# Optimization experiments

Hardware: AMD Instinct MI355X
Metric: run time of the kernel (lower is better)

## Reference

```python
import jax, jax.numpy as jnp
import numpy as np

NUM_TOKENS = 8192
D_MODEL = 512
D_FF = 1024
NUM_EXPERTS = 8
TOP_K = 2


def setup_inputs() -> dict:
    key = jax.random.key(0)
    k_x, k_r, k_w1, k_w2 = jax.random.split(key, 4)
    x = jax.random.normal(k_x, (NUM_TOKENS, D_MODEL), dtype=jnp.float32)
    # Router weight [num_experts, d_model]
    w_router = jax.random.normal(k_r, (NUM_EXPERTS, D_MODEL), dtype=jnp.float32) * 0.02
    # Expert weights stored as [E, N, K] (kernel convention: y = x @ W.T)
    w1 = jax.random.normal(k_w1, (NUM_EXPERTS, D_FF, D_MODEL), dtype=jnp.float32) * 0.02
    w2 = jax.random.normal(k_w2, (NUM_EXPERTS, D_MODEL, D_FF), dtype=jnp.float32) * 0.02
    return {"x": x, "w_router": w_router, "w1": w1, "w2": w2}


def reference(x, w_router, w1, w2):
    # Router: softmax over experts, top-k selection, renormalized gates
    logits = jnp.einsum("td,ed->te", x, w_router)            # [T, E]
    probs = jax.nn.softmax(logits, axis=-1)
    top_vals, top_idx = jax.lax.top_k(probs, TOP_K)           # [T, k]
    top_vals = top_vals / jnp.sum(top_vals, axis=-1, keepdims=True)

    # Combine weights per (token, expert): topk weight if selected else 0.
    # out[t] = sum_e gate[t,e] * W2[e] @ silu(W1[e] @ x[t])
    out = jnp.zeros_like(x)
    for e in range(NUM_EXPERTS):
        gate_e = jnp.sum(jnp.where(top_idx == e, top_vals, 0.0), axis=-1)  # [T]
        h = jax.nn.silu(jnp.einsum("td,fd->tf", x, w1[e]))                 # [T, d_ff]
        y = jnp.einsum("tf,df->td", h, w2[e])                              # [T, d]
        out = out + gate_e[:, None] * y
    return out
```

## Files before the change

### kernel.cpp

```cpp
#include <hip/hip_runtime.h>
#include <hip/hip_bf16.h>

#define NT 8192
#define DM 512
#define DF 1024
#define NE 8
#define MAXROWS (NT*2)

typedef __bf16 bf16_8 __attribute__((ext_vector_type(8)));
typedef float  f32_4  __attribute__((ext_vector_type(4)));
typedef unsigned short us8 __attribute__((ext_vector_type(8)));

__device__ inline unsigned short f2bf(float f) {
    unsigned int u = __float_as_uint(f);
    u = u + 0x7fffu + ((u >> 16) & 1u);
    return (unsigned short)(u >> 16);
}

__device__ inline bf16_8 as_bf(us8 v) { return __builtin_bit_cast(bf16_8, v); }

__device__ inline void gld16(const unsigned short* g, unsigned short* l) {
    __builtin_amdgcn_global_load_lds(
        (const __attribute__((address_space(1))) unsigned int*)g,
        (__attribute__((address_space(3))) unsigned int*)l, 16, 0, 0);
}

__global__ __launch_bounds__(256) void cast_kernel(const float* __restrict__ in,
                                                   unsigned short* __restrict__ out,
                                                   int n4) {
    int i = blockIdx.x * 256 + threadIdx.x;
    if (i >= n4) return;
    float4 v = ((const float4*)in)[i];
    ushort4 o;
    o.x = f2bf(v.x); o.y = f2bf(v.y); o.z = f2bf(v.z); o.w = f2bf(v.w);
    ((ushort4*)out)[i] = o;
}

__global__ __launch_bounds__(256) void router_kernel(const float* __restrict__ x,
                                                     const float* __restrict__ wr,
                                                     int* __restrict__ eidx,
                                                     float2* __restrict__ gates) {
    const int wid = threadIdx.x >> 6;
    const int lane = threadIdx.x & 63;
    const int t = blockIdx.x * 4 + wid;

    const float4* xrow = (const float4*)(x + (size_t)t * DM);
    float4 xv0 = xrow[lane * 2];
    float4 xv1 = xrow[lane * 2 + 1];

    float logit[NE];
#pragma unroll
    for (int e = 0; e < NE; ++e) {
        const float4* wrow = (const float4*)(wr + (size_t)e * DM);
        float4 w0 = wrow[lane * 2];
        float4 w1v = wrow[lane * 2 + 1];
        float s = xv0.x * w0.x + xv0.y * w0.y + xv0.z * w0.z + xv0.w * w0.w
                + xv1.x * w1v.x + xv1.y * w1v.y + xv1.z * w1v.z + xv1.w * w1v.w;
#pragma unroll
        for (int off = 32; off >= 1; off >>= 1) s += __shfl_xor(s, off);
        logit[e] = s;
    }

    if (lane == 0) {
        int i0 = 0; float m0 = logit[0];
#pragma unroll
        for (int e = 1; e < NE; ++e) if (logit[e] > m0) { m0 = logit[e]; i0 = e; }
        int i1 = -1; float m1 = -1e30f;
#pragma unroll
        for (int e = 0; e < NE; ++e) if (e != i0 && logit[e] > m1) { m1 = logit[e]; i1 = e; }
        float d = expf(m1 - m0);
        float g0 = 1.0f / (1.0f + d);
        float g1 = 1.0f - g0;
        eidx[t] = i0 | (i1 << 8);
        gates[t] = make_float2(g0, g1);
    }
}

__global__ __launch_bounds__(256) void build_lists_kernel(const int* __restrict__ eidx,
                                                          const float2* __restrict__ gates,
                                                          int* __restrict__ counts,
                                                          int* __restrict__ token_list,
                                                          float* __restrict__ gate_list) {
    const int e = blockIdx.x;
    const int tid = threadIdx.x;
    const int wid = tid >> 6, lane = tid & 63;
    __shared__ int wsum[4];
    __shared__ int base;
    if (tid == 0) base = 0;
    __syncthreads();
    for (int c = 0; c < NT; c += 256) {
        int t = c + tid;
        int ei = eidx[t];
        int i0 = ei & 0xff, i1 = (ei >> 8) & 0xff;
        bool match0 = (i0 == e), match1 = (i1 == e);
        bool m = match0 || match1;
        unsigned long long mask = __ballot(m);
        if (lane == 0) wsum[wid] = __popcll(mask);
        __syncthreads();
        int pre = 0;
#pragma unroll
        for (int w = 0; w < 4; ++w) if (w < wid) pre += wsum[w];
        int tot = wsum[0] + wsum[1] + wsum[2] + wsum[3];
        if (m) {
            int pos = base + pre + __popcll(mask & ((1ULL << lane) - 1ULL));
            token_list[e * NT + pos] = t;
            float2 g = gates[t];
            gate_list[e * NT + pos] = match0 ? g.x : g.y;
        }
        __syncthreads();
        if (tid == 0) base += tot;
        __syncthreads();
    }
    if (tid == 0) counts[e] = base;
}

__global__ void scan_kernel(const int* __restrict__ counts, int* __restrict__ offsets) {
    if (threadIdx.x == 0) {
        int s = 0;
        for (int e = 0; e < NE; ++e) { offsets[e] = s; s += counts[e]; }
    }
}

template <bool G1>
__global__ __launch_bounds__(256) void moe_gemm(const unsigned short* __restrict__ Abase,
                                                const unsigned short* __restrict__ Wbase,
                                                unsigned short* __restrict__ h_out,
                                                float* __restrict__ out,
                                                const int* __restrict__ counts,
                                                const int* __restrict__ offsets,
                                                const int* __restrict__ token_list,
                                                const float* __restrict__ gate_list) {
    constexpr int K = G1 ? DM : DF;
    constexpr int NCOLS = G1 ? DF : DM;
    const int e = blockIdx.z;
    const int cnt = counts[e];
    const int row0 = blockIdx.y * 128;
    if (row0 >= cnt) return;
    const int col0 = blockIdx.x * 128;
    const int off_e = offsets[e];

    __shared__ __align__(16) unsigned short Alds[128 * 32];
    __shared__ __align__(16) unsigned short Blds[128 * 32];

    const int tid = threadIdx.x;
    const int wid = tid >> 6;
    const int lane = tid & 63;

    const int c0 = wid * 128 + lane;
    const int c1 = c0 + 64;
    const int r0 = c0 >> 2, q0 = c0 & 3;
    const int r1 = c1 >> 2, q1 = c1 & 3;
    const int qs0 = q0 ^ (r0 & 3);
    const int qs1 = q1 ^ (r1 & 3);

    const unsigned short* gA0;
    const unsigned short* gA1;
    {
        int rr0 = min(row0 + r0, cnt - 1);
        int rr1 = min(row0 + r1, cnt - 1);
        if (G1) {
            gA0 = Abase + (size_t)token_list[e * NT + rr0] * K + qs0 * 8;
            gA1 = Abase + (size_t)token_list[e * NT + rr1] * K + qs1 * 8;
        } else {
            gA0 = Abase + (size_t)(off_e + rr0) * K + qs0 * 8;
            gA1 = Abase + (size_t)(off_e + rr1) * K + qs1 * 8;
        }
    }
    const unsigned short* gB0 = Wbase + ((size_t)e * NCOLS + col0 + r0) * K + qs0 * 8;
    const unsigned short* gB1 = Wbase + ((size_t)e * NCOLS + col0 + r1) * K + qs1 * 8;

    unsigned short* ldsA0 = Alds + (wid * 128) * 8;
    unsigned short* ldsA1 = Alds + (wid * 128 + 64) * 8;
    unsigned short* ldsB0 = Blds + (wid * 128) * 8;
    unsigned short* ldsB1 = Blds + (wid * 128 + 64) * 8;

    const int wr = wid >> 1, wc = wid & 1;
    const int lrow = lane & 15;
    const int kcs = (lane >> 4) ^ (lrow & 3);
    const unsigned short* rdA[4];
    const unsigned short* rdB[4];
#pragma unroll
    for (int m = 0; m < 4; ++m)
        rdA[m] = Alds + (wr * 64 + m * 16 + lrow) * 32 + kcs * 8;
#pragma unroll
    for (int n = 0; n < 4; ++n)
        rdB[n] = Blds + (wc * 64 + n * 16 + lrow) * 32 + kcs * 8;

    f32_4 acc[4][4];
#pragma unroll
    for (int m = 0; m < 4; ++m)
#pragma unroll
        for (int n = 0; n < 4; ++n) acc[m][n] = (f32_4){0.f, 0.f, 0.f, 0.f};

    for (int k0 = 0; k0 < K; k0 += 32) {
        gld16(gA0 + k0, ldsA0);
        gld16(gA1 + k0, ldsA1);
        gld16(gB0 + k0, ldsB0);
        gld16(gB1 + k0, ldsB1);
        __syncthreads();

        bf16_8 a[4], b[4];
#pragma unroll
        for (int m = 0; m < 4; ++m) a[m] = as_bf(*(const us8*)rdA[m]);
#pragma unroll
        for (int n = 0; n < 4; ++n) b[n] = as_bf(*(const us8*)rdB[n]);
#pragma unroll
        for (int m = 0; m < 4; ++m)
#pragma unroll
            for (int n = 0; n < 4; ++n)
                acc[m][n] = __builtin_amdgcn_mfma_f32_16x16x32_bf16(a[m], b[n], acc[m][n], 0, 0, 0);
        __syncthreads();
    }

#pragma unroll
    for (int m = 0; m < 4; ++m) {
#pragma unroll
        for (int n = 0; n < 4; ++n) {
#pragma unroll
            for (int q = 0; q < 4; ++q) {
                int lr = wr * 64 + m * 16 + (lane >> 4) * 4 + q;
                int lc = wc * 64 + n * 16 + (lane & 15);
                int r = row0 + lr;
                if (r < cnt) {
                    float v = acc[m][n][q];
                    if (G1) {
                        v = v / (1.0f + expf(-v));
                        h_out[(size_t)(off_e + r) * DF + col0 + lc] = f2bf(v);
                    } else {
                        float g = gate_list[e * NT + r];
                        int tok = token_list[e * NT + r];
                        atomicAdd(&out[(size_t)tok * DM + col0 + lc], g * v);
                    }
                }
            }
        }
    }
}

extern "C" void kernel_launch(void* const* d_in, const int* in_sizes, int n_in,
                              void* d_out, int out_size, void* d_ws, size_t ws_size,
                              hipStream_t stream) {
    const float* x   = (const float*)d_in[0];
    const float* wrt = (const float*)d_in[1];
    const float* w1  = (const float*)d_in[2];
    const float* w2  = (const float*)d_in[3];
    float* out = (float*)d_out;

    char* ws = (char*)d_ws;
    size_t o = 0;
    auto alloc = [&](size_t bytes) { size_t r = o; o += (bytes + 255) & ~255UL; return r; };
    unsigned short* x_bf  = (unsigned short*)(ws + alloc((size_t)NT * DM * 2));
    unsigned short* w1_bf = (unsigned short*)(ws + alloc((size_t)NE * DF * DM * 2));
    unsigned short* w2_bf = (unsigned short*)(ws + alloc((size_t)NE * DM * DF * 2));
    unsigned short* h_bf  = (unsigned short*)(ws + alloc((size_t)MAXROWS * DF * 2));
    int*   counts     = (int*)(ws + alloc(NE * 4));
    int*   offsets    = (int*)(ws + alloc(NE * 4));
    int*   token_list = (int*)(ws + alloc((size_t)NE * NT * 4));
    float* gate_list  = (float*)(ws + alloc((size_t)NE * NT * 4));
    int*   eidx       = (int*)(ws + alloc((size_t)NT * 4));
    float2* gates     = (float2*)(ws + alloc((size_t)NT * 8));

    hipMemsetAsync(out, 0, (size_t)NT * DM * 4, stream);

    int n4x = NT * DM / 4;
    cast_kernel<<<(n4x + 255) / 256, 256, 0, stream>>>(x, x_bf, n4x);
    int n4w = NE * DF * DM / 4;
    cast_kernel<<<(n4w + 255) / 256, 256, 0, stream>>>(w1, w1_bf, n4w);
    cast_kernel<<<(n4w + 255) / 256, 256, 0, stream>>>(w2, w2_bf, n4w);

    router_kernel<<<NT / 4, 256, 0, stream>>>(x, wrt, eidx, gates);
    build_lists_kernel<<<NE, 256, 0, stream>>>(eidx, gates, counts, token_list, gate_list);
    scan_kernel<<<1, 64, 0, stream>>>(counts, offsets);

    moe_gemm<true><<<dim3(DF / 128, NT / 128, NE), 256, 0, stream>>>(
        x_bf, w1_bf, h_bf, nullptr, counts, offsets, token_list, gate_list);
    moe_gemm<false><<<dim3(DM / 128, NT / 128, NE), 256, 0, stream>>>(
        h_bf, w2_bf, nullptr, out, counts, offsets, token_list, gate_list);
}
```

Baseline: 164.5 us.

## Double-buffer LDS tiles in MoE GEMM to overlap global loads with MFMA

Adds a second LDS buffer for the A and B tiles. The next k-step's global-to-LDS loads are issued before computing on the current buffer, and manual vmcnt/lgkmcnt waits plus raw s_barrier replace __syncthreads. It also sets launch_bounds occupancy to 4 blocks per CU. The aim is to hide global memory latency behind the MFMA work. In exchange it doubles LDS use and adds register pressure under the occupancy hint.

```diff
diff --git a/kernel.cpp b/kernel.cpp
--- a/kernel.cpp
+++ b/kernel.cpp
@@ -122,16 +122,18 @@
 }
 
 template <bool G1>
-__global__ __launch_bounds__(256) void moe_gemm(const unsigned short* __restrict__ Abase,
-                                                const unsigned short* __restrict__ Wbase,
-                                                unsigned short* __restrict__ h_out,
-                                                float* __restrict__ out,
-                                                const int* __restrict__ counts,
-                                                const int* __restrict__ offsets,
-                                                const int* __restrict__ token_list,
-                                                const float* __restrict__ gate_list) {
+__global__ __launch_bounds__(256, 4) void moe_gemm(const unsigned short* __restrict__ Abase,
+                                                   const unsigned short* __restrict__ Wbase,
+                                                   unsigned short* __restrict__ h_out,
+                                                   float* __restrict__ out,
+                                                   const int* __restrict__ counts,
+                                                   const int* __restrict__ offsets,
+                                                   const int* __restrict__ token_list,
+                                                   const float* __restrict__ gate_list) {
     constexpr int K = G1 ? DM : DF;
     constexpr int NCOLS = G1 ? DF : DM;
+    constexpr int NSTEP = K / 32;
+    constexpr int TILE_E = 128 * 32;
     const int e = blockIdx.z;
     const int cnt = counts[e];
     const int row0 = blockIdx.y * 128;
@@ -139,8 +141,8 @@
     const int col0 = blockIdx.x * 128;
     const int off_e = offsets[e];
 
-    __shared__ __align__(16) unsigned short Alds[128 * 32];
-    __shared__ __align__(16) unsigned short Blds[128 * 32];
+    __shared__ __align__(16) unsigned short Alds[2 * TILE_E];
+    __shared__ __align__(16) unsigned short Blds[2 * TILE_E];
 
     const int tid = threadIdx.x;
     const int wid = tid >> 6;
@@ -169,22 +171,19 @@
     const unsigned short* gB0 = Wbase + ((size_t)e * NCOLS + col0 + r0) * K + qs0 * 8;
     const unsigned short* gB1 = Wbase + ((size_t)e * NCOLS + col0 + r1) * K + qs1 * 8;
 
-    unsigned short* ldsA0 = Alds + (wid * 128) * 8;
-    unsigned short* ldsA1 = Alds + (wid * 128 + 64) * 8;
-    unsigned short* ldsB0 = Blds + (wid * 128) * 8;
-    unsigned short* ldsB1 = Blds + (wid * 128 + 64) * 8;
+    const int ldsOff0 = (wid * 128) * 8;
+    const int ldsOff1 = (wid * 128 + 64) * 8;
 
     const int wr = wid >> 1, wc = wid & 1;
     const int lrow = lane & 15;
     const int kcs = (lane >> 4) ^ (lrow & 3);
-    const unsigned short* rdA[4];
-    const unsigned short* rdB[4];
+    int offA[4], offB[4];
 #pragma unroll
     for (int m = 0; m < 4; ++m)
-        rdA[m] = Alds + (wr * 64 + m * 16 + lrow) * 32 + kcs * 8;
+        offA[m] = (wr * 64 + m * 16 + lrow) * 32 + kcs * 8;
 #pragma unroll
     for (int n = 0; n < 4; ++n)
-        rdB[n] = Blds + (wc * 64 + n * 16 + lrow) * 32 + kcs * 8;
+        offB[n] = (wc * 64 + n * 16 + lrow) * 32 + kcs * 8;
 
     f32_4 acc[4][4];
 #pragma unroll
@@ -192,24 +191,45 @@
 #pragma unroll
         for (int n = 0; n < 4; ++n) acc[m][n] = (f32_4){0.f, 0.f, 0.f, 0.f};
 
-    for (int k0 = 0; k0 < K; k0 += 32) {
-        gld16(gA0 + k0, ldsA0);
-        gld16(gA1 + k0, ldsA1);
-        gld16(gB0 + k0, ldsB0);
-        gld16(gB1 + k0, ldsB1);
-        __syncthreads();
-
+    auto issue = [&](int t) {
+        int bb = t & 1;
+        unsigned short* A_l = Alds + bb * TILE_E;
+        unsigned short* B_l = Blds + bb * TILE_E;
+        int k0 = t * 32;
+        gld16(gA0 + k0, A_l + ldsOff0);
+        gld16(gA1 + k0, A_l + ldsOff1);
+        gld16(gB0 + k0, B_l + ldsOff0);
+        gld16(gB1 + k0, B_l + ldsOff1);
+    };
+
+    issue(0);
+#pragma unroll 2
+    for (int t = 0; t < NSTEP; ++t) {
+        if (t + 1 < NSTEP) {
+            issue(t + 1);
+            asm volatile("s_waitcnt vmcnt(4)" ::: "memory");
+        } else {
+            asm volatile("s_waitcnt vmcnt(0)" ::: "memory");
+        }
+        __builtin_amdgcn_sched_barrier(0);
+        __builtin_amdgcn_s_barrier();
+
+        const unsigned short* A_l = Alds + (t & 1) * TILE_E;
+        const unsigned short* B_l = Blds + (t & 1) * TILE_E;
         bf16_8 a[4], b[4];
 #pragma unroll
-        for (int m = 0; m < 4; ++m) a[m] = as_bf(*(const us8*)rdA[m]);
-#pragma unroll
-        for (int n = 0; n < 4; ++n) b[n] = as_bf(*(const us8*)rdB[n]);
+        for (int m = 0; m < 4; ++m) a[m] = as_bf(*(const us8*)(A_l + offA[m]));
+#pragma unroll
+        for (int n = 0; n < 4; ++n) b[n] = as_bf(*(const us8*)(B_l + offB[n]));
 #pragma unroll
         for (int m = 0; m < 4; ++m)
 #pragma unroll
             for (int n = 0; n < 4; ++n)
                 acc[m][n] = __builtin_amdgcn_mfma_f32_16x16x32_bf16(a[m], b[n], acc[m][n], 0, 0, 0);
-        __syncthreads();
+
+        asm volatile("s_waitcnt lgkmcnt(0)" ::: "memory");
+        __builtin_amdgcn_sched_barrier(0);
+        __builtin_amdgcn_s_barrier();
     }
 
 #pragma unroll
```

Result: slower. 169.0 us (+2.7%).
